# Performance work log

Hardware: AMD Instinct MI355X
Metric: run time of the kernel (lower is better)

Reference implementation:

```python
import jax, jax.numpy as jnp
import numpy as np

N_NODES = 100000
N_EDGES = 3200000
D_IN = 128
H1 = 32
H2 = 64
N_CLASSES = 10
N_GRAPHS = 64


def setup_inputs() -> dict:
    key = jax.random.key(0)
    ks = jax.random.split(key, 10)
    x = jax.random.normal(ks[0], (N_NODES, D_IN), dtype=jnp.float32)
    edge_index = jax.random.randint(ks[1], (2, N_EDGES), 0, N_NODES, dtype=jnp.int64)
    batch = jnp.sort(jax.random.randint(ks[2], (N_NODES,), 0, N_GRAPHS, dtype=jnp.int64))
    # torch Linear params: weight [out, in], bias [out]
    W1 = jax.random.normal(ks[3], (H1, D_IN), dtype=jnp.float32) * (1.0 / np.sqrt(D_IN))
    b1 = jnp.zeros((H1,), dtype=jnp.float32)
    W2 = jax.random.normal(ks[4], (H2, H1), dtype=jnp.float32) * (1.0 / np.sqrt(H1))
    b2 = jnp.zeros((H2,), dtype=jnp.float32)
    Wf = jax.random.normal(ks[5], (N_CLASSES, H2), dtype=jnp.float32) * (1.0 / np.sqrt(H2))
    bf = jnp.zeros((N_CLASSES,), dtype=jnp.float32)
    return {"x": x, "edge_index": edge_index, "batch": batch,
            "W1": W1, "b1": b1, "W2": W2, "b2": b2, "Wf": Wf, "bf": bf}


def _graph_conv(h, row, col, n_nodes, W, b):
    # h: [N, F_in] -> lin -> gather x_j from row (source), scatter-add to col (target)
    h = h @ W.T + b  # [N, F_out]
    deg = jax.ops.segment_sum(jnp.ones(row.shape[0], h.dtype), row, num_segments=n_nodes)
    dis = deg ** -0.5  # self-loops guarantee deg >= 1
    norm = dis[row] * dis[col]  # [E]
    msg = norm[:, None] * h[row]  # gather-multiply, [E, F_out]
    return jax.ops.segment_sum(msg, col, num_segments=n_nodes)  # scatter-add


def reference(x, edge_index, batch, W1, b1, W2, b2, Wf, bf):
    n = x.shape[0]
    loops = jnp.arange(n, dtype=edge_index.dtype)
    ei = jnp.concatenate([edge_index, jnp.stack([loops, loops])], axis=1)  # add_self_loops
    row, col = ei[0], ei[1]
    h = jax.nn.relu(_graph_conv(x, row, col, n, W1, b1))
    h = jax.nn.relu(_graph_conv(h, row, col, n, W2, b2))
    # global_mean_pool over graph ids
    sums = jax.ops.segment_sum(h, batch, num_segments=N_GRAPHS)  # [G, H2]
    counts = jax.ops.segment_sum(jnp.ones(n, h.dtype), batch, num_segments=N_GRAPHS)
    pooled = sums / jnp.maximum(counts, 1.0)[:, None]
    logits = pooled @ Wf.T + bf
    return jax.nn.softmax(logits, axis=1)
```

## Files before the change

### kernel.cpp

```cpp
#include <hip/hip_runtime.h>

#define N_NODES   100000
#define N_EDGES   3200000
#define D_IN      128
#define H1F       32
#define H2F       64
#define N_CLASSES 10
#define N_GRAPHS  64

#define NBUCK 391
#define CAP   10240
#define RCAP  10240
#define EPB   3072
#define NPB   ((N_EDGES + EPB - 1) / EPB)

__device__ __forceinline__ unsigned f2bf(float f) {
    unsigned u = __float_as_uint(f);
    return (u + 0x7fffu + ((u >> 16) & 1u)) >> 16;
}
__device__ __forceinline__ float bf2f(unsigned h) {
    return __uint_as_float(h << 16);
}

__global__ __launch_bounds__(256) void k_part(const int* __restrict__ row,
        const int* __restrict__ col, int* cpos, int* rpos,
        unsigned* __restrict__ partc, unsigned char* __restrict__ partr) {
    __shared__ int sc[512], sr[512];
    __shared__ int posc[NBUCK], posr[NBUCK];
    __shared__ int basec[NBUCK], baser[NBUCK];
    __shared__ unsigned stagc[EPB];
    __shared__ unsigned char stagr[EPB];
    __shared__ unsigned short stagcb[EPB];
    __shared__ unsigned short stagrb[EPB];
    int t = threadIdx.x;
    sc[t] = 0; sc[t + 256] = 0; sr[t] = 0; sr[t + 256] = 0;
    __syncthreads();
    int s = blockIdx.x * EPB;
    int e = min(s + EPB, N_EDGES);
    for (int i = s + t; i < e; i += 256) {
        atomicAdd(&sc[col[i] >> 8], 1);
        atomicAdd(&sr[row[i] >> 8], 1);
    }
    __syncthreads();
    for (int o = 1; o < 512; o <<= 1) {
        int a0 = (t >= o) ? sc[t - o] : 0;
        int a1 = sc[t + 256 - o];
        int b0 = (t >= o) ? sr[t - o] : 0;
        int b1 = sr[t + 256 - o];
        __syncthreads();
        sc[t] += a0; sc[t + 256] += a1;
        sr[t] += b0; sr[t + 256] += b1;
        __syncthreads();
    }
    for (int b = t; b < NBUCK; b += 256) {
        int cc = sc[b] - (b ? sc[b - 1] : 0);
        int rc = sr[b] - (b ? sr[b - 1] : 0);
        posc[b] = sc[b] - cc;
        posr[b] = sr[b] - rc;
        basec[b] = cc ? (b * CAP + atomicAdd(&cpos[b], cc)) : 0;
        baser[b] = rc ? (b * RCAP + atomicAdd(&rpos[b], rc)) : 0;
    }
    __syncthreads();
    for (int i = s + t; i < e; i += 256) {
        int c = col[i], r = row[i];
        int b = c >> 8;
        int p = atomicAdd(&posc[b], 1);
        stagc[p] = ((unsigned)(c & 255) << 17) | (unsigned)r;
        stagcb[p] = (unsigned short)b;
        int b2 = r >> 8;
        int p2 = atomicAdd(&posr[b2], 1);
        stagr[p2] = (unsigned char)(r & 255);
        stagrb[p2] = (unsigned short)b2;
    }
    __syncthreads();
    int nloc = e - s;
    for (int i = t; i < nloc; i += 256) {
        int b = stagcb[i];
        int start = b ? sc[b - 1] : 0;
        partc[basec[b] + (i - start)] = stagc[i];
    }
    for (int i = t; i < nloc; i += 256) {
        int b = stagrb[i];
        int start = b ? sr[b - 1] : 0;
        partr[baser[b] + (i - start)] = stagr[i];
    }
}

__global__ __launch_bounds__(256) void k_buckets(const unsigned* __restrict__ partc,
        const unsigned char* __restrict__ partr, const int* __restrict__ cpos,
        const int* __restrict__ rpos, int2* __restrict__ srcoff,
        int* __restrict__ srcw, float* __restrict__ dis) {
    int t = threadIdx.x;
    if (blockIdx.x < NBUCK) {
        __shared__ int cnt[256], sc[256], run[256];
        int b = blockIdx.x;
        cnt[t] = 0; run[t] = 0;
        __syncthreads();
        int s = b * CAP, e = s + cpos[b];
        for (int i = s + t; i < e; i += 256)
            atomicAdd(&cnt[partc[i] >> 17], 1);
        __syncthreads();
        int v = cnt[t]; sc[t] = v; __syncthreads();
        for (int o = 1; o < 256; o <<= 1) {
            int a = (t >= o) ? sc[t - o] : 0;
            __syncthreads();
            sc[t] += a;
            __syncthreads();
        }
        int ex = sc[t] - v;
        __syncthreads();
        sc[t] = ex;
        __syncthreads();
        int n = (b << 8) + t;
        if (n < N_NODES) srcoff[n] = make_int2(s + ex, s + ex + v);
        for (int i = s + t; i < e; i += 256) {
            unsigned p = partc[i];
            int c = p >> 17;
            int k = atomicAdd(&run[c], 1);
            srcw[s + sc[c] + k] = (int)(p & 0x1FFFFu);
        }
    } else {
        __shared__ int cnt[256];
        int b = blockIdx.x - NBUCK;
        cnt[t] = 0;
        __syncthreads();
        int s = b * RCAP, e = s + rpos[b];
        for (int i = s + t; i < e; i += 256) atomicAdd(&cnt[partr[i]], 1);
        __syncthreads();
        int n = (b << 8) + t;
        if (n < N_NODES) dis[n] = rsqrtf((float)(1 + cnt[t]));
    }
}

__global__ __launch_bounds__(256) void k_lin1(const float* __restrict__ x,
        const float* __restrict__ W1, const float* __restrict__ b1,
        const float* __restrict__ dis, unsigned* __restrict__ hs1b) {
    __shared__ float w1t[D_IN][H1F + 1];
    __shared__ float xs[8][D_IN];
    int tid = threadIdx.x;
    for (int idx = tid; idx < H1F * D_IN; idx += 256) {
        int f = idx >> 7, k = idx & 127;
        w1t[k][f] = W1[idx];
    }
    int nbase = blockIdx.x * 8;
    for (int idx = tid; idx < 8 * D_IN; idx += 256) {
        int nn = idx >> 7, k = idx & 127;
        int n = nbase + nn;
        xs[nn][k] = (n < N_NODES) ? x[(long long)n * D_IN + k] : 0.0f;
    }
    __syncthreads();
    int f = tid & 31, sub = tid >> 5;
    int n = nbase + sub;
    float acc = 0.f;
    #pragma unroll
    for (int k = 0; k < D_IN; ++k) acc += xs[sub][k] * w1t[k][f];
    float val = (n < N_NODES) ? dis[n] * (acc + b1[f]) : 0.f;
    float other = __shfl_xor(val, 1);
    if ((f & 1) == 0 && n < N_NODES)
        hs1b[n * 16 + (f >> 1)] = f2bf(val) | (f2bf(other) << 16);
}

__global__ __launch_bounds__(256) void k_gather1(const int* __restrict__ srcw,
        const int2* __restrict__ srcoff, const float* __restrict__ dis,
        const unsigned* __restrict__ hs, unsigned* __restrict__ out) {
    int lane = threadIdx.x & 63;
    int c = (blockIdx.x * 256 + threadIdx.x) >> 6;
    if (c >= N_NODES) return;
    int e8 = lane >> 3, l8 = lane & 7;
    int2 so = srcoff[c];
    int s = so.x, e = so.y;
    float a0 = 0.f, a1 = 0.f, a2 = 0.f, a3 = 0.f;
    if (e8 == 0) {
        uint2 u = ((const uint2*)(hs + c * 16))[l8];
        a0 = bf2f(u.x & 0xffffu); a1 = bf2f(u.x >> 16);
        a2 = bf2f(u.y & 0xffffu); a3 = bf2f(u.y >> 16);
    }
    int j = s + e8;
    for (; j + 8 < e; j += 16) {
        int s0 = srcw[j], s1 = srcw[j + 8];
        uint2 u0 = ((const uint2*)(hs + s0 * 16))[l8];
        uint2 u1 = ((const uint2*)(hs + s1 * 16))[l8];
        a0 += bf2f(u0.x & 0xffffu); a1 += bf2f(u0.x >> 16);
        a2 += bf2f(u0.y & 0xffffu); a3 += bf2f(u0.y >> 16);
        a0 += bf2f(u1.x & 0xffffu); a1 += bf2f(u1.x >> 16);
        a2 += bf2f(u1.y & 0xffffu); a3 += bf2f(u1.y >> 16);
    }
    if (j < e) {
        uint2 u0 = ((const uint2*)(hs + srcw[j] * 16))[l8];
        a0 += bf2f(u0.x & 0xffffu); a1 += bf2f(u0.x >> 16);
        a2 += bf2f(u0.y & 0xffffu); a3 += bf2f(u0.y >> 16);
    }
    a0 += __shfl_xor(a0, 8);  a1 += __shfl_xor(a1, 8);
    a2 += __shfl_xor(a2, 8);  a3 += __shfl_xor(a3, 8);
    a0 += __shfl_xor(a0, 16); a1 += __shfl_xor(a1, 16);
    a2 += __shfl_xor(a2, 16); a3 += __shfl_xor(a3, 16);
    a0 += __shfl_xor(a0, 32); a1 += __shfl_xor(a1, 32);
    a2 += __shfl_xor(a2, 32); a3 += __shfl_xor(a3, 32);
    if (e8 == 0) {
        float dc = dis[c];
        uint2 w;
        w.x = f2bf(dc * fmaxf(dc * a0, 0.f)) | (f2bf(dc * fmaxf(dc * a1, 0.f)) << 16);
        w.y = f2bf(dc * fmaxf(dc * a2, 0.f)) | (f2bf(dc * fmaxf(dc * a3, 0.f)) << 16);
        ((uint2*)(out + c * 16))[l8] = w;
    }
}

__global__ __launch_bounds__(256) void k_gather2(const int* __restrict__ srcw,
        const int2* __restrict__ srcoff, const float* __restrict__ dis,
        const unsigned* __restrict__ hs, float* __restrict__ G,
        float* __restrict__ Sd) {
    int lane = threadIdx.x & 63;
    int c = (blockIdx.x * 256 + threadIdx.x) >> 6;
    if (c >= N_NODES) return;
    int e8 = lane >> 3, l8 = lane & 7;
    int2 so = srcoff[c];
    int s = so.x, e = so.y;
    float a0 = 0.f, a1 = 0.f, a2 = 0.f, a3 = 0.f, ad = 0.f;
    if (e8 == 0) {
        uint2 u = ((const uint2*)(hs + c * 16))[l8];
        a0 = bf2f(u.x & 0xffffu); a1 = bf2f(u.x >> 16);
        a2 = bf2f(u.y & 0xffffu); a3 = bf2f(u.y >> 16);
    }
    int j = s + e8;
    for (; j + 8 < e; j += 16) {
        int s0 = srcw[j], s1 = srcw[j + 8];
        uint2 u0 = ((const uint2*)(hs + s0 * 16))[l8];
        uint2 u1 = ((const uint2*)(hs + s1 * 16))[l8];
        if (l8 == 0) ad += dis[s0] + dis[s1];
        a0 += bf2f(u0.x & 0xffffu); a1 += bf2f(u0.x >> 16);
        a2 += bf2f(u0.y & 0xffffu); a3 += bf2f(u0.y >> 16);
        a0 += bf2f(u1.x & 0xffffu); a1 += bf2f(u1.x >> 16);
        a2 += bf2f(u1.y & 0xffffu); a3 += bf2f(u1.y >> 16);
    }
    if (j < e) {
        int s0 = srcw[j];
        uint2 u0 = ((const uint2*)(hs + s0 * 16))[l8];
        if (l8 == 0) ad += dis[s0];
        a0 += bf2f(u0.x & 0xffffu); a1 += bf2f(u0.x >> 16);
        a2 += bf2f(u0.y & 0xffffu); a3 += bf2f(u0.y >> 16);
    }
    a0 += __shfl_xor(a0, 8);  a1 += __shfl_xor(a1, 8);
    a2 += __shfl_xor(a2, 8);  a3 += __shfl_xor(a3, 8);
    ad += __shfl_xor(ad, 8);
    a0 += __shfl_xor(a0, 16); a1 += __shfl_xor(a1, 16);
    a2 += __shfl_xor(a2, 16); a3 += __shfl_xor(a3, 16);
    ad += __shfl_xor(ad, 16);
    a0 += __shfl_xor(a0, 32); a1 += __shfl_xor(a1, 32);
    a2 += __shfl_xor(a2, 32); a3 += __shfl_xor(a3, 32);
    ad += __shfl_xor(ad, 32);
    if (e8 == 0) {
        float dc = dis[c];
        float4 w; w.x = dc * a0; w.y = dc * a1; w.z = dc * a2; w.w = dc * a3;
        *(float4*)(&G[c * 32 + l8 * 4]) = w;
        if (l8 == 0) Sd[c] = dc * (dc + ad);
    }
}

__global__ __launch_bounds__(256) void k_lin2pool(const float* __restrict__ G,
        const float* __restrict__ Sd, const float* __restrict__ W2,
        const float* __restrict__ b2, const int* __restrict__ batch,
        float* __restrict__ sums) {
    __shared__ float w2t[H1F][H2F + 1];
    int tid = threadIdx.x;
    for (int idx = tid; idx < H2F * H1F; idx += 256) {
        int fo = idx >> 5, k = idx & 31;
        w2t[k][fo] = W2[idx];
    }
    __syncthreads();
    int f = tid & 63, sub = tid >> 6;
    float bfv = b2[f];
    int n0 = blockIdx.x * 256;
    float acc = 0.f; int gcur = -1;
    for (int i = sub; i < 256; i += 4) {
        int n = n0 + i;
        if (n >= N_NODES) break;
        const float4* Gr = (const float4*)(&G[n * 32]);
        float d = Sd[n] * bfv;
        #pragma unroll
        for (int q = 0; q < 8; ++q) {
            float4 v = Gr[q];
            d += v.x * w2t[4 * q][f] + v.y * w2t[4 * q + 1][f]
               + v.z * w2t[4 * q + 2][f] + v.w * w2t[4 * q + 3][f];
        }
        d = fmaxf(d, 0.f);
        int gg = batch[n];
        if (gg != gcur) {
            if (gcur >= 0) atomicAdd(&sums[gcur * H2F + f], acc);
            acc = 0.f; gcur = gg;
        }
        acc += d;
    }
    if (gcur >= 0) atomicAdd(&sums[gcur * H2F + f], acc);
}

__global__ __launch_bounds__(640) void k_final(const float* __restrict__ sums,
        const int* __restrict__ batch, const float* __restrict__ Wf,
        const float* __restrict__ bf, float* __restrict__ out) {
    __shared__ float l[N_GRAPHS * N_CLASSES];
    __shared__ float cnts[N_GRAPHS];
    int tid = threadIdx.x;
    if (tid < N_GRAPHS) {
        int g = tid;
        int lo = 0, hi = N_NODES;
        while (lo < hi) { int mid = (lo + hi) >> 1; if (batch[mid] < g) lo = mid + 1; else hi = mid; }
        int start = lo;
        hi = N_NODES;
        while (lo < hi) { int mid = (lo + hi) >> 1; if (batch[mid] < g + 1) lo = mid + 1; else hi = mid; }
        cnts[g] = (float)(lo - start);
    }
    __syncthreads();
    if (tid < N_GRAPHS * N_CLASSES) {
        int g = tid / N_CLASSES, c = tid % N_CLASSES;
        float cnt = fmaxf(cnts[g], 1.0f);
        float acc = bf[c];
        for (int f = 0; f < H2F; ++f)
            acc += (sums[g * H2F + f] / cnt) * Wf[c * H2F + f];
        l[tid] = acc;
    }
    __syncthreads();
    if (tid < N_GRAPHS) {
        float m = -1e30f;
        for (int c = 0; c < N_CLASSES; ++c) m = fmaxf(m, l[tid * N_CLASSES + c]);
        float s = 0.f;
        float ex[N_CLASSES];
        for (int c = 0; c < N_CLASSES; ++c) { ex[c] = expf(l[tid * N_CLASSES + c] - m); s += ex[c]; }
        for (int c = 0; c < N_CLASSES; ++c) out[tid * N_CLASSES + c] = ex[c] / s;
    }
}

extern "C" void kernel_launch(void* const* d_in, const int* in_sizes, int n_in,
                              void* d_out, int out_size, void* d_ws, size_t ws_size,
                              hipStream_t stream) {
    const float* x     = (const float*)d_in[0];
    const int*   ei    = (const int*)d_in[1];
    const int*   batch = (const int*)d_in[2];
    const float* W1    = (const float*)d_in[3];
    const float* b1    = (const float*)d_in[4];
    const float* W2    = (const float*)d_in[5];
    const float* b2    = (const float*)d_in[6];
    const float* Wf    = (const float*)d_in[7];
    const float* bf    = (const float*)d_in[8];
    float* out = (float*)d_out;

    const int* row = ei;
    const int* col = ei + N_EDGES;

    int* W = (int*)d_ws;
    int*           cpos   = W + 0;
    int*           rpos   = W + 400;
    float*         sums   = (float*)(W + 800);
    int2*          srcoff = (int2*)(W + 4904);
    int*           srcw   = W + 204904;
    unsigned*      partc  = (unsigned*)(W + 4208744);
    float*         G      = (float*)(W + 4208744);
    unsigned char* partr  = (unsigned char*)(W + 8212584);
    float*         dis    = (float*)(W + 9213544);
    float*         Sd     = (float*)(W + 9313544);
    unsigned*      hs1b   = (unsigned*)(W + 9413544);
    unsigned*      hs2b   = (unsigned*)(W + 11013544);

    hipMemsetAsync(W, 0, (800 + N_GRAPHS * H2F) * sizeof(int), stream);

    k_part<<<NPB, 256, 0, stream>>>(row, col, cpos, rpos, partc, partr);
    k_buckets<<<2 * NBUCK, 256, 0, stream>>>(partc, partr, cpos, rpos, srcoff, srcw, dis);

    k_lin1<<<(N_NODES + 7) / 8, 256, 0, stream>>>(x, W1, b1, dis, hs1b);
    k_gather1<<<(N_NODES + 3) / 4, 256, 0, stream>>>(srcw, srcoff, dis, hs1b, hs2b);

    k_gather2<<<(N_NODES + 3) / 4, 256, 0, stream>>>(srcw, srcoff, dis, hs2b, G, Sd);

    k_lin2pool<<<(N_NODES + 255) / 256, 256, 0, stream>>>(G, Sd, W2, b2, batch, sums);
    k_final<<<1, 640, 0, stream>>>(sums, batch, Wf, bf, out);
}
```

Baseline: 314.9 us.

## Fuse second-layer gather with linear and mean-pool; unroll gather loops by four

Merges the second aggregation kernel with the W2 linear and pooling kernel. Each wavefront now processes 16 consecutive nodes, reduces neighbor features, applies W2 through wave shuffles, and accumulates pooled sums in registers before issuing atomics. This drops the G and Sd intermediate buffers and one kernel launch. Both gather loops are also unrolled to four loads in flight per lane. The trade-off is fewer, longer-running wavefronts: only about 1563 blocks, and the nodes within each wave are processed one after another, which may hurt latency hiding.

```diff
diff --git a/kernel.cpp b/kernel.cpp
--- a/kernel.cpp
+++ b/kernel.cpp
@@ -13,6 +13,7 @@
 #define RCAP  10240
 #define EPB   3072
 #define NPB   ((N_EDGES + EPB - 1) / EPB)
+#define NPW   16
 
 __device__ __forceinline__ unsigned f2bf(float f) {
     unsigned u = __float_as_uint(f);
@@ -176,16 +177,22 @@
         a2 = bf2f(u.y & 0xffffu); a3 = bf2f(u.y >> 16);
     }
     int j = s + e8;
-    for (; j + 8 < e; j += 16) {
-        int s0 = srcw[j], s1 = srcw[j + 8];
+    for (; j + 24 < e; j += 32) {
+        int s0 = srcw[j], s1 = srcw[j + 8], s2 = srcw[j + 16], s3 = srcw[j + 24];
         uint2 u0 = ((const uint2*)(hs + s0 * 16))[l8];
         uint2 u1 = ((const uint2*)(hs + s1 * 16))[l8];
+        uint2 u2 = ((const uint2*)(hs + s2 * 16))[l8];
+        uint2 u3 = ((const uint2*)(hs + s3 * 16))[l8];
         a0 += bf2f(u0.x & 0xffffu); a1 += bf2f(u0.x >> 16);
         a2 += bf2f(u0.y & 0xffffu); a3 += bf2f(u0.y >> 16);
         a0 += bf2f(u1.x & 0xffffu); a1 += bf2f(u1.x >> 16);
         a2 += bf2f(u1.y & 0xffffu); a3 += bf2f(u1.y >> 16);
-    }
-    if (j < e) {
+        a0 += bf2f(u2.x & 0xffffu); a1 += bf2f(u2.x >> 16);
+        a2 += bf2f(u2.y & 0xffffu); a3 += bf2f(u2.y >> 16);
+        a0 += bf2f(u3.x & 0xffffu); a1 += bf2f(u3.x >> 16);
+        a2 += bf2f(u3.y & 0xffffu); a3 += bf2f(u3.y >> 16);
+    }
+    for (; j < e; j += 8) {
         uint2 u0 = ((const uint2*)(hs + srcw[j] * 16))[l8];
         a0 += bf2f(u0.x & 0xffffu); a1 += bf2f(u0.x >> 16);
         a2 += bf2f(u0.y & 0xffffu); a3 += bf2f(u0.y >> 16);
@@ -205,59 +212,9 @@
     }
 }
 
-__global__ __launch_bounds__(256) void k_gather2(const int* __restrict__ srcw,
+__global__ __launch_bounds__(256) void k_g2pool(const int* __restrict__ srcw,
         const int2* __restrict__ srcoff, const float* __restrict__ dis,
-        const unsigned* __restrict__ hs, float* __restrict__ G,
-        float* __restrict__ Sd) {
-    int lane = threadIdx.x & 63;
-    int c = (blockIdx.x * 256 + threadIdx.x) >> 6;
-    if (c >= N_NODES) return;
-    int e8 = lane >> 3, l8 = lane & 7;
-    int2 so = srcoff[c];
-    int s = so.x, e = so.y;
-    float a0 = 0.f, a1 = 0.f, a2 = 0.f, a3 = 0.f, ad = 0.f;
-    if (e8 == 0) {
-        uint2 u = ((const uint2*)(hs + c * 16))[l8];
-        a0 = bf2f(u.x & 0xffffu); a1 = bf2f(u.x >> 16);
-        a2 = bf2f(u.y & 0xffffu); a3 = bf2f(u.y >> 16);
-    }
-    int j = s + e8;
-    for (; j + 8 < e; j += 16) {
-        int s0 = srcw[j], s1 = srcw[j + 8];
-        uint2 u0 = ((const uint2*)(hs + s0 * 16))[l8];
-        uint2 u1 = ((const uint2*)(hs + s1 * 16))[l8];
-        if (l8 == 0) ad += dis[s0] + dis[s1];
-        a0 += bf2f(u0.x & 0xffffu); a1 += bf2f(u0.x >> 16);
-        a2 += bf2f(u0.y & 0xffffu); a3 += bf2f(u0.y >> 16);
-        a0 += bf2f(u1.x & 0xffffu); a1 += bf2f(u1.x >> 16);
-        a2 += bf2f(u1.y & 0xffffu); a3 += bf2f(u1.y >> 16);
-    }
-    if (j < e) {
-        int s0 = srcw[j];
-        uint2 u0 = ((const uint2*)(hs + s0 * 16))[l8];
-        if (l8 == 0) ad += dis[s0];
-        a0 += bf2f(u0.x & 0xffffu); a1 += bf2f(u0.x >> 16);
-        a2 += bf2f(u0.y & 0xffffu); a3 += bf2f(u0.y >> 16);
-    }
-    a0 += __shfl_xor(a0, 8);  a1 += __shfl_xor(a1, 8);
-    a2 += __shfl_xor(a2, 8);  a3 += __shfl_xor(a3, 8);
-    ad += __shfl_xor(ad, 8);
-    a0 += __shfl_xor(a0, 16); a1 += __shfl_xor(a1, 16);
-    a2 += __shfl_xor(a2, 16); a3 += __shfl_xor(a3, 16);
-    ad += __shfl_xor(ad, 16);
-    a0 += __shfl_xor(a0, 32); a1 += __shfl_xor(a1, 32);
-    a2 += __shfl_xor(a2, 32); a3 += __shfl_xor(a3, 32);
-    ad += __shfl_xor(ad, 32);
-    if (e8 == 0) {
-        float dc = dis[c];
-        float4 w; w.x = dc * a0; w.y = dc * a1; w.z = dc * a2; w.w = dc * a3;
-        *(float4*)(&G[c * 32 + l8 * 4]) = w;
-        if (l8 == 0) Sd[c] = dc * (dc + ad);
-    }
-}
-
-__global__ __launch_bounds__(256) void k_lin2pool(const float* __restrict__ G,
-        const float* __restrict__ Sd, const float* __restrict__ W2,
+        const unsigned* __restrict__ hs, const float* __restrict__ W2,
         const float* __restrict__ b2, const int* __restrict__ batch,
         float* __restrict__ sums) {
     __shared__ float w2t[H1F][H2F + 1];
@@ -267,23 +224,72 @@
         w2t[k][fo] = W2[idx];
     }
     __syncthreads();
-    int f = tid & 63, sub = tid >> 6;
-    float bfv = b2[f];
-    int n0 = blockIdx.x * 256;
+    int wv = tid >> 6, lane = tid & 63;
+    int e8 = lane >> 3, l8 = lane & 7;
+    int f = lane;
+    float b2f = b2[f];
+    int c0 = (blockIdx.x * 4 + wv) * NPW;
     float acc = 0.f; int gcur = -1;
-    for (int i = sub; i < 256; i += 4) {
-        int n = n0 + i;
-        if (n >= N_NODES) break;
-        const float4* Gr = (const float4*)(&G[n * 32]);
-        float d = Sd[n] * bfv;
+    for (int i = 0; i < NPW; ++i) {
+        int c = c0 + i;
+        if (c >= N_NODES) break;
+        int2 so = srcoff[c];
+        int s = so.x, e = so.y;
+        float a0 = 0.f, a1 = 0.f, a2 = 0.f, a3 = 0.f, ad = 0.f;
+        if (e8 == 0) {
+            uint2 u = ((const uint2*)(hs + c * 16))[l8];
+            a0 = bf2f(u.x & 0xffffu); a1 = bf2f(u.x >> 16);
+            a2 = bf2f(u.y & 0xffffu); a3 = bf2f(u.y >> 16);
+        }
+        int j = s + e8;
+        for (; j + 24 < e; j += 32) {
+            int s0 = srcw[j], s1 = srcw[j + 8], s2 = srcw[j + 16], s3 = srcw[j + 24];
+            uint2 u0 = ((const uint2*)(hs + s0 * 16))[l8];
+            uint2 u1 = ((const uint2*)(hs + s1 * 16))[l8];
+            uint2 u2 = ((const uint2*)(hs + s2 * 16))[l8];
+            uint2 u3 = ((const uint2*)(hs + s3 * 16))[l8];
+            if (l8 == 0) ad += (dis[s0] + dis[s1]) + (dis[s2] + dis[s3]);
+            a0 += bf2f(u0.x & 0xffffu); a1 += bf2f(u0.x >> 16);
+            a2 += bf2f(u0.y & 0xffffu); a3 += bf2f(u0.y >> 16);
+            a0 += bf2f(u1.x & 0xffffu); a1 += bf2f(u1.x >> 16);
+            a2 += bf2f(u1.y & 0xffffu); a3 += bf2f(u1.y >> 16);
+            a0 += bf2f(u2.x & 0xffffu); a1 += bf2f(u2.x >> 16);
+            a2 += bf2f(u2.y & 0xffffu); a3 += bf2f(u2.y >> 16);
+            a0 += bf2f(u3.x & 0xffffu); a1 += bf2f(u3.x >> 16);
+            a2 += bf2f(u3.y & 0xffffu); a3 += bf2f(u3.y >> 16);
+        }
+        for (; j < e; j += 8) {
+            int s0 = srcw[j];
+            uint2 u0 = ((const uint2*)(hs + s0 * 16))[l8];
+            if (l8 == 0) ad += dis[s0];
+            a0 += bf2f(u0.x & 0xffffu); a1 += bf2f(u0.x >> 16);
+            a2 += bf2f(u0.y & 0xffffu); a3 += bf2f(u0.y >> 16);
+        }
+        a0 += __shfl_xor(a0, 8);  a1 += __shfl_xor(a1, 8);
+        a2 += __shfl_xor(a2, 8);  a3 += __shfl_xor(a3, 8);
+        ad += __shfl_xor(ad, 8);
+        a0 += __shfl_xor(a0, 16); a1 += __shfl_xor(a1, 16);
+        a2 += __shfl_xor(a2, 16); a3 += __shfl_xor(a3, 16);
+        ad += __shfl_xor(ad, 16);
+        a0 += __shfl_xor(a0, 32); a1 += __shfl_xor(a1, 32);
+        a2 += __shfl_xor(a2, 32); a3 += __shfl_xor(a3, 32);
+        ad += __shfl_xor(ad, 32);
+        float dc = dis[c];
+        float sd = dc * (dc + ad);
+        float dot = 0.f;
         #pragma unroll
-        for (int q = 0; q < 8; ++q) {
-            float4 v = Gr[q];
-            d += v.x * w2t[4 * q][f] + v.y * w2t[4 * q + 1][f]
-               + v.z * w2t[4 * q + 2][f] + v.w * w2t[4 * q + 3][f];
-        }
-        d = fmaxf(d, 0.f);
-        int gg = batch[n];
+        for (int k = 0; k < H1F; ++k) {
+            float gk;
+            switch (k & 3) {
+                case 0: gk = __shfl(a0, k >> 2); break;
+                case 1: gk = __shfl(a1, k >> 2); break;
+                case 2: gk = __shfl(a2, k >> 2); break;
+                default: gk = __shfl(a3, k >> 2); break;
+            }
+            dot += gk * w2t[k][f];
+        }
+        float d = fmaxf(sd * b2f + dc * dot, 0.f);
+        int gg = batch[c];
         if (gg != gcur) {
             if (gcur >= 0) atomicAdd(&sums[gcur * H2F + f], acc);
             acc = 0.f; gcur = gg;
@@ -352,12 +358,10 @@
     int2*          srcoff = (int2*)(W + 4904);
     int*           srcw   = W + 204904;
     unsigned*      partc  = (unsigned*)(W + 4208744);
-    float*         G      = (float*)(W + 4208744);
     unsigned char* partr  = (unsigned char*)(W + 8212584);
     float*         dis    = (float*)(W + 9213544);
-    float*         Sd     = (float*)(W + 9313544);
-    unsigned*      hs1b   = (unsigned*)(W + 9413544);
-    unsigned*      hs2b   = (unsigned*)(W + 11013544);
+    unsigned*      hs1b   = (unsigned*)(W + 9313544);
+    unsigned*      hs2b   = (unsigned*)(W + 10913544);
 
     hipMemsetAsync(W, 0, (800 + N_GRAPHS * H2F) * sizeof(int), stream);
 
@@ -367,8 +371,8 @@
     k_lin1<<<(N_NODES + 7) / 8, 256, 0, stream>>>(x, W1, b1, dis, hs1b);
     k_gather1<<<(N_NODES + 3) / 4, 256, 0, stream>>>(srcw, srcoff, dis, hs1b, hs2b);
 
-    k_gather2<<<(N_NODES + 3) / 4, 256, 0, stream>>>(srcw, srcoff, dis, hs2b, G, Sd);
-
-    k_lin2pool<<<(N_NODES + 255) / 256, 256, 0, stream>>>(G, Sd, W2, b2, batch, sums);
+    k_g2pool<<<(N_NODES + 4 * NPW - 1) / (4 * NPW), 256, 0, stream>>>(
+        srcw, srcoff, dis, hs2b, W2, b2, batch, sums);
+
     k_final<<<1, 640, 0, stream>>>(sums, batch, Wf, bf, out);
 }
```

After: 332.1 us. 5.5% more time.

## Split bf16 feature tables into halves and gather each half separately

Applied to the files above, without the earlier changes.

The 32-feature bf16 node table is split into two 16-feature halves (lo/hi), and each gather pass runs twice, once per half. Each half-table is 3.2 MB, small enough to stay resident in cache during the random gathers. The cost is reading the edge list twice per layer and issuing extra kernel launches. The gather loops are also unrolled to four edges per lane-group, and edge indices are read with nontemporal loads.

```diff
diff --git a/kernel.cpp b/kernel.cpp
--- a/kernel.cpp
+++ b/kernel.cpp
@@ -134,7 +134,8 @@
 
 __global__ __launch_bounds__(256) void k_lin1(const float* __restrict__ x,
         const float* __restrict__ W1, const float* __restrict__ b1,
-        const float* __restrict__ dis, unsigned* __restrict__ hs1b) {
+        const float* __restrict__ dis, unsigned* __restrict__ hs1lo,
+        unsigned* __restrict__ hs1hi) {
     __shared__ float w1t[D_IN][H1F + 1];
     __shared__ float xs[8][D_IN];
     int tid = threadIdx.x;
@@ -156,103 +157,106 @@
     for (int k = 0; k < D_IN; ++k) acc += xs[sub][k] * w1t[k][f];
     float val = (n < N_NODES) ? dis[n] * (acc + b1[f]) : 0.f;
     float other = __shfl_xor(val, 1);
-    if ((f & 1) == 0 && n < N_NODES)
-        hs1b[n * 16 + (f >> 1)] = f2bf(val) | (f2bf(other) << 16);
-}
-
-__global__ __launch_bounds__(256) void k_gather1(const int* __restrict__ srcw,
+    if ((f & 1) == 0 && n < N_NODES) {
+        unsigned packed = f2bf(val) | (f2bf(other) << 16);
+        unsigned* dst = (f < 16) ? hs1lo : hs1hi;
+        dst[n * 8 + ((f & 15) >> 1)] = packed;
+    }
+}
+
+__global__ __launch_bounds__(256) void k_gather1h(const int* __restrict__ srcw,
         const int2* __restrict__ srcoff, const float* __restrict__ dis,
-        const unsigned* __restrict__ hs, unsigned* __restrict__ out) {
+        const unsigned* __restrict__ tab, unsigned* __restrict__ outh) {
     int lane = threadIdx.x & 63;
     int c = (blockIdx.x * 256 + threadIdx.x) >> 6;
     if (c >= N_NODES) return;
     int e8 = lane >> 3, l8 = lane & 7;
     int2 so = srcoff[c];
     int s = so.x, e = so.y;
-    float a0 = 0.f, a1 = 0.f, a2 = 0.f, a3 = 0.f;
+    float a0 = 0.f, a1 = 0.f;
     if (e8 == 0) {
-        uint2 u = ((const uint2*)(hs + c * 16))[l8];
-        a0 = bf2f(u.x & 0xffffu); a1 = bf2f(u.x >> 16);
-        a2 = bf2f(u.y & 0xffffu); a3 = bf2f(u.y >> 16);
+        unsigned u = tab[c * 8 + l8];
+        a0 = bf2f(u & 0xffffu); a1 = bf2f(u >> 16);
     }
     int j = s + e8;
-    for (; j + 8 < e; j += 16) {
-        int s0 = srcw[j], s1 = srcw[j + 8];
-        uint2 u0 = ((const uint2*)(hs + s0 * 16))[l8];
-        uint2 u1 = ((const uint2*)(hs + s1 * 16))[l8];
-        a0 += bf2f(u0.x & 0xffffu); a1 += bf2f(u0.x >> 16);
-        a2 += bf2f(u0.y & 0xffffu); a3 += bf2f(u0.y >> 16);
-        a0 += bf2f(u1.x & 0xffffu); a1 += bf2f(u1.x >> 16);
-        a2 += bf2f(u1.y & 0xffffu); a3 += bf2f(u1.y >> 16);
-    }
-    if (j < e) {
-        uint2 u0 = ((const uint2*)(hs + srcw[j] * 16))[l8];
-        a0 += bf2f(u0.x & 0xffffu); a1 += bf2f(u0.x >> 16);
-        a2 += bf2f(u0.y & 0xffffu); a3 += bf2f(u0.y >> 16);
+    for (; j + 24 < e; j += 32) {
+        int s0 = __builtin_nontemporal_load(srcw + j);
+        int s1 = __builtin_nontemporal_load(srcw + j + 8);
+        int s2 = __builtin_nontemporal_load(srcw + j + 16);
+        int s3 = __builtin_nontemporal_load(srcw + j + 24);
+        unsigned u0 = tab[s0 * 8 + l8];
+        unsigned u1 = tab[s1 * 8 + l8];
+        unsigned u2 = tab[s2 * 8 + l8];
+        unsigned u3 = tab[s3 * 8 + l8];
+        a0 += bf2f(u0 & 0xffffu); a1 += bf2f(u0 >> 16);
+        a0 += bf2f(u1 & 0xffffu); a1 += bf2f(u1 >> 16);
+        a0 += bf2f(u2 & 0xffffu); a1 += bf2f(u2 >> 16);
+        a0 += bf2f(u3 & 0xffffu); a1 += bf2f(u3 >> 16);
+    }
+    for (; j < e; j += 8) {
+        int s0 = __builtin_nontemporal_load(srcw + j);
+        unsigned u0 = tab[s0 * 8 + l8];
+        a0 += bf2f(u0 & 0xffffu); a1 += bf2f(u0 >> 16);
     }
     a0 += __shfl_xor(a0, 8);  a1 += __shfl_xor(a1, 8);
-    a2 += __shfl_xor(a2, 8);  a3 += __shfl_xor(a3, 8);
     a0 += __shfl_xor(a0, 16); a1 += __shfl_xor(a1, 16);
-    a2 += __shfl_xor(a2, 16); a3 += __shfl_xor(a3, 16);
     a0 += __shfl_xor(a0, 32); a1 += __shfl_xor(a1, 32);
-    a2 += __shfl_xor(a2, 32); a3 += __shfl_xor(a3, 32);
     if (e8 == 0) {
         float dc = dis[c];
-        uint2 w;
-        w.x = f2bf(dc * fmaxf(dc * a0, 0.f)) | (f2bf(dc * fmaxf(dc * a1, 0.f)) << 16);
-        w.y = f2bf(dc * fmaxf(dc * a2, 0.f)) | (f2bf(dc * fmaxf(dc * a3, 0.f)) << 16);
-        ((uint2*)(out + c * 16))[l8] = w;
-    }
-}
-
-__global__ __launch_bounds__(256) void k_gather2(const int* __restrict__ srcw,
+        outh[c * 8 + l8] = f2bf(dc * fmaxf(dc * a0, 0.f))
+                         | (f2bf(dc * fmaxf(dc * a1, 0.f)) << 16);
+    }
+}
+
+template<bool WSD>
+__global__ __launch_bounds__(256) void k_gather2h(const int* __restrict__ srcw,
         const int2* __restrict__ srcoff, const float* __restrict__ dis,
-        const unsigned* __restrict__ hs, float* __restrict__ G,
-        float* __restrict__ Sd) {
+        const unsigned* __restrict__ tab, float* __restrict__ G,
+        float* __restrict__ Sd, int fbase) {
     int lane = threadIdx.x & 63;
     int c = (blockIdx.x * 256 + threadIdx.x) >> 6;
     if (c >= N_NODES) return;
     int e8 = lane >> 3, l8 = lane & 7;
     int2 so = srcoff[c];
     int s = so.x, e = so.y;
-    float a0 = 0.f, a1 = 0.f, a2 = 0.f, a3 = 0.f, ad = 0.f;
+    float a0 = 0.f, a1 = 0.f, ad = 0.f;
     if (e8 == 0) {
-        uint2 u = ((const uint2*)(hs + c * 16))[l8];
-        a0 = bf2f(u.x & 0xffffu); a1 = bf2f(u.x >> 16);
-        a2 = bf2f(u.y & 0xffffu); a3 = bf2f(u.y >> 16);
+        unsigned u = tab[c * 8 + l8];
+        a0 = bf2f(u & 0xffffu); a1 = bf2f(u >> 16);
     }
     int j = s + e8;
-    for (; j + 8 < e; j += 16) {
-        int s0 = srcw[j], s1 = srcw[j + 8];
-        uint2 u0 = ((const uint2*)(hs + s0 * 16))[l8];
-        uint2 u1 = ((const uint2*)(hs + s1 * 16))[l8];
-        if (l8 == 0) ad += dis[s0] + dis[s1];
-        a0 += bf2f(u0.x & 0xffffu); a1 += bf2f(u0.x >> 16);
-        a2 += bf2f(u0.y & 0xffffu); a3 += bf2f(u0.y >> 16);
-        a0 += bf2f(u1.x & 0xffffu); a1 += bf2f(u1.x >> 16);
-        a2 += bf2f(u1.y & 0xffffu); a3 += bf2f(u1.y >> 16);
-    }
-    if (j < e) {
-        int s0 = srcw[j];
-        uint2 u0 = ((const uint2*)(hs + s0 * 16))[l8];
-        if (l8 == 0) ad += dis[s0];
-        a0 += bf2f(u0.x & 0xffffu); a1 += bf2f(u0.x >> 16);
-        a2 += bf2f(u0.y & 0xffffu); a3 += bf2f(u0.y >> 16);
+    for (; j + 24 < e; j += 32) {
+        int s0 = __builtin_nontemporal_load(srcw + j);
+        int s1 = __builtin_nontemporal_load(srcw + j + 8);
+        int s2 = __builtin_nontemporal_load(srcw + j + 16);
+        int s3 = __builtin_nontemporal_load(srcw + j + 24);
+        unsigned u0 = tab[s0 * 8 + l8];
+        unsigned u1 = tab[s1 * 8 + l8];
+        unsigned u2 = tab[s2 * 8 + l8];
+        unsigned u3 = tab[s3 * 8 + l8];
+        if (WSD && l8 == 0) ad += (dis[s0] + dis[s1]) + (dis[s2] + dis[s3]);
+        a0 += bf2f(u0 & 0xffffu); a1 += bf2f(u0 >> 16);
+        a0 += bf2f(u1 & 0xffffu); a1 += bf2f(u1 >> 16);
+        a0 += bf2f(u2 & 0xffffu); a1 += bf2f(u2 >> 16);
+        a0 += bf2f(u3 & 0xffffu); a1 += bf2f(u3 >> 16);
+    }
+    for (; j < e; j += 8) {
+        int s0 = __builtin_nontemporal_load(srcw + j);
+        unsigned u0 = tab[s0 * 8 + l8];
+        if (WSD && l8 == 0) ad += dis[s0];
+        a0 += bf2f(u0 & 0xffffu); a1 += bf2f(u0 >> 16);
     }
     a0 += __shfl_xor(a0, 8);  a1 += __shfl_xor(a1, 8);
-    a2 += __shfl_xor(a2, 8);  a3 += __shfl_xor(a3, 8);
-    ad += __shfl_xor(ad, 8);
     a0 += __shfl_xor(a0, 16); a1 += __shfl_xor(a1, 16);
-    a2 += __shfl_xor(a2, 16); a3 += __shfl_xor(a3, 16);
-    ad += __shfl_xor(ad, 16);
     a0 += __shfl_xor(a0, 32); a1 += __shfl_xor(a1, 32);
-    a2 += __shfl_xor(a2, 32); a3 += __shfl_xor(a3, 32);
-    ad += __shfl_xor(ad, 32);
+    if (WSD) {
+        ad += __shfl_xor(ad, 8); ad += __shfl_xor(ad, 16); ad += __shfl_xor(ad, 32);
+    }
     if (e8 == 0) {
         float dc = dis[c];
-        float4 w; w.x = dc * a0; w.y = dc * a1; w.z = dc * a2; w.w = dc * a3;
-        *(float4*)(&G[c * 32 + l8 * 4]) = w;
-        if (l8 == 0) Sd[c] = dc * (dc + ad);
+        float2 w; w.x = dc * a0; w.y = dc * a1;
+        *(float2*)(&G[c * 32 + fbase + l8 * 2]) = w;
+        if (WSD && l8 == 0) Sd[c] = dc * (dc + ad);
     }
 }
 
@@ -356,18 +360,22 @@
     unsigned char* partr  = (unsigned char*)(W + 8212584);
     float*         dis    = (float*)(W + 9213544);
     float*         Sd     = (float*)(W + 9313544);
-    unsigned*      hs1b   = (unsigned*)(W + 9413544);
-    unsigned*      hs2b   = (unsigned*)(W + 11013544);
+    unsigned*      hs1lo  = (unsigned*)(W + 9413544);
+    unsigned*      hs1hi  = (unsigned*)(W + 10213544);
+    unsigned*      hs2lo  = (unsigned*)(W + 11013544);
+    unsigned*      hs2hi  = (unsigned*)(W + 11813544);
 
     hipMemsetAsync(W, 0, (800 + N_GRAPHS * H2F) * sizeof(int), stream);
 
     k_part<<<NPB, 256, 0, stream>>>(row, col, cpos, rpos, partc, partr);
     k_buckets<<<2 * NBUCK, 256, 0, stream>>>(partc, partr, cpos, rpos, srcoff, srcw, dis);
 
-    k_lin1<<<(N_NODES + 7) / 8, 256, 0, stream>>>(x, W1, b1, dis, hs1b);
-    k_gather1<<<(N_NODES + 3) / 4, 256, 0, stream>>>(srcw, srcoff, dis, hs1b, hs2b);
-
-    k_gather2<<<(N_NODES + 3) / 4, 256, 0, stream>>>(srcw, srcoff, dis, hs2b, G, Sd);
+    k_lin1<<<(N_NODES + 7) / 8, 256, 0, stream>>>(x, W1, b1, dis, hs1lo, hs1hi);
+    k_gather1h<<<(N_NODES + 3) / 4, 256, 0, stream>>>(srcw, srcoff, dis, hs1lo, hs2lo);
+    k_gather1h<<<(N_NODES + 3) / 4, 256, 0, stream>>>(srcw, srcoff, dis, hs1hi, hs2hi);
+
+    k_gather2h<true><<<(N_NODES + 3) / 4, 256, 0, stream>>>(srcw, srcoff, dis, hs2lo, G, Sd, 0);
+    k_gather2h<false><<<(N_NODES + 3) / 4, 256, 0, stream>>>(srcw, srcoff, dis, hs2hi, G, Sd, 16);
 
     k_lin2pool<<<(N_NODES + 255) / 256, 256, 0, stream>>>(G, Sd, W2, b2, batch, sums);
     k_final<<<1, 640, 0, stream>>>(sums, batch, Wf, bf, out);
```

After: 408.3 us. 29.7% more time.
